# Optimization experiments

Hardware: AMD Instinct MI355X
Metric: run time of the kernel (lower is better)

## Reference

```python
import jax, jax.numpy as jnp
import numpy as np

BETA = 0.95
THR = 1.0
T = 50        # NUM_TIME_STEPS
L = 2         # SNN_NUM_LAYERS
SLOPE = 25.0  # fast_sigmoid surrogate slope

@jax.custom_vjp
def spike(v):
    # Heaviside on (mem - threshold) with fast_sigmoid surrogate gradient
    return (v > 0).astype(v.dtype)

def _spike_fwd(v):
    return (v > 0).astype(v.dtype), v

def _spike_bwd(v, g):
    return (g / (SLOPE * jnp.abs(v) + 1.0) ** 2,)

spike.defvjp(_spike_fwd, _spike_bwd)


def setup_inputs() -> dict:
    key = jax.random.key(0)
    k1, k2, _ = jax.random.split(key, 3)
    B, IN, H = 4096, 512, 1024
    x = jax.random.normal(k1, (B, IN), dtype=jnp.float32)
    W_proj = jax.random.normal(k2, (IN, H), dtype=jnp.float32) / np.sqrt(IN).astype(np.float32)
    b_proj = jnp.zeros((H,), dtype=jnp.float32)
    return {"x": x, "W_proj": W_proj, "b_proj": b_proj}


def reference(x, W_proj, b_proj):
    # Static input current fed at every time step (input_features != hidden -> Linear projection)
    inp = x @ W_proj + b_proj                         # [B, H]
    B, H = inp.shape

    def step(carry, _):
        mems, agg, tot = carry
        new_mems = []
        for li in range(L):  # independent LIF layers, all driven by the same static input
            mem = mems[li]
            # snnTorch Leaky (reset_mechanism='subtract'):
            reset = spike(mem - THR)                  # reset based on previous mem
            mem = BETA * mem + inp - reset * THR      # leaky integration + subtractive reset
            spk = spike(mem - THR)                    # output spike from new mem
            new_mems.append(mem)
            tot = tot + spk.sum(axis=1)               # total spikes per sample (all layers)
            if li == L - 1:
                agg = agg + spk                       # sum of last-layer spikes over time
        return (tuple(new_mems), agg, tot), None

    init = (
        tuple(jnp.zeros((B, H), inp.dtype) for _ in range(L)),  # init_leaky -> zeros
        jnp.zeros((B, H), inp.dtype),
        jnp.zeros((B,), inp.dtype),
    )
    (mems, agg, tot), _ = jax.lax.scan(step, init, None, length=T)
    return agg, tot
```

## Files before the change

kernel.cpp:

```cpp
#include <hip/hip_runtime.h>
#include <stdint.h>

#define MDIM 4096
#define NDIM 1024
#define KDIM 512
#define TSTEPS 50
#define NCH 16

typedef _Float16 half8 __attribute__((ext_vector_type(8)));
typedef float    f32x4 __attribute__((ext_vector_type(4)));

typedef const __attribute__((address_space(1))) void cgv_t;
typedef __attribute__((address_space(3))) void lv_t;

__device__ __forceinline__ void gload16(const void* g, void* s) {
    __builtin_amdgcn_global_load_lds((cgv_t*)g, (lv_t*)s, 16, 0, 0);
}

__global__ __launch_bounds__(256) void split_kernel(
    const float* __restrict__ A, const float* __restrict__ W,
    char* __restrict__ A1, char* __restrict__ A2,
    char* __restrict__ B1, char* __restrict__ B2,
    float* __restrict__ tot)
{
    const int blk = blockIdx.x;
    if (blk < 1024) {
        int idx = blk * 256 + threadIdx.x;
        if (idx < MDIM) tot[idx] = 0.0f;
        int r = idx >> 6, q = idx & 63, c = q >> 2, lg = q & 3;
        const float* pA = A + (size_t)r * KDIM + c * 32 + lg * 8;
        float4 v0 = *(const float4*)pA;
        float4 v1 = *(const float4*)(pA + 4);
        float v[8] = {v0.x, v0.y, v0.z, v0.w, v1.x, v1.y, v1.z, v1.w};
        half8 h1, h2;
        #pragma unroll
        for (int e = 0; e < 8; ++e) {
            h1[e] = (_Float16)v[e];
            h2[e] = (_Float16)((v[e] - (float)h1[e]) * 2048.0f);
        }
        int off = (r >> 6) * 65536 + c * 4096 + lg * 1024
                + (((r & 63) ^ (lg << 1)) << 4);
        *(half8*)(A1 + off) = h1;
        *(half8*)(A2 + off) = h2;
    } else {
        int idx = (blk - 1024) * 256 + threadIdx.x;
        int q = idx >> 10, n = idx & 1023, c = q >> 2, lg = q & 3;
        float v[8];
        #pragma unroll
        for (int e = 0; e < 8; ++e)
            v[e] = W[(size_t)(c * 32 + lg * 8 + e) * NDIM + n];
        half8 h1, h2;
        #pragma unroll
        for (int e = 0; e < 8; ++e) {
            h1[e] = (_Float16)v[e];
            h2[e] = (_Float16)((v[e] - (float)h1[e]) * 2048.0f);
        }
        int off = (n >> 6) * 65536 + c * 4096 + lg * 1024
                + (((n & 63) ^ (lg << 1)) << 4);
        *(half8*)(B1 + off) = h1;
        *(half8*)(B2 + off) = h2;
    }
}

__global__ __launch_bounds__(256, 4) void snn_mfma_kernel(
    const char* __restrict__ A1, const char* __restrict__ A2,
    const char* __restrict__ B1, const char* __restrict__ B2,
    const float* __restrict__ bias, float* __restrict__ agg, float* __restrict__ tot)
{
    __shared__ __align__(16) unsigned char lds[2][16384];

    const int t  = threadIdx.x;
    const int l  = t & 63;
    const int w  = t >> 6;
    const int li = l & 15;
    const int lg = l >> 4;
    const int qr = (w >> 1) * 32;
    const int qc = (w & 1) * 32;

    const int swz = (blockIdx.x & 7) * 128 + (blockIdx.x >> 3);
    const int m0 = (swz >> 4) * 64;
    const int n0 = (swz & 15) * 64;

    const int aoff = (m0 >> 6) * 65536 + w * 1024 + l * 16;
    const int boff = (n0 >> 6) * 65536 + w * 1024 + l * 16;
    const int dstw = w * 1024;

#define STAGE(buf, ch) do {                                                   \
    const int c_ = (ch) * 4096;                                               \
    gload16(A1 + aoff + c_, &lds[buf][dstw]);                                 \
    gload16(A2 + aoff + c_, &lds[buf][4096  + dstw]);                         \
    gload16(B1 + boff + c_, &lds[buf][8192  + dstw]);                         \
    gload16(B2 + boff + c_, &lds[buf][12288 + dstw]);                         \
} while (0)

    int aL[2], bL[2];
    #pragma unroll
    for (int i = 0; i < 2; ++i) {
        aL[i] = lg * 1024 + (((qr + i * 16 + li) ^ (lg << 1)) << 4);
        bL[i] = lg * 1024 + (((qc + i * 16 + li) ^ (lg << 1)) << 4);
    }

    f32x4 acc_lo[2][2], acc_hi[2][2];
    #pragma unroll
    for (int i = 0; i < 2; ++i)
        #pragma unroll
        for (int j = 0; j < 2; ++j) {
            acc_lo[i][j] = (f32x4){0.f, 0.f, 0.f, 0.f};
            acc_hi[i][j] = (f32x4){0.f, 0.f, 0.f, 0.f};
        }

    STAGE(0, 0);
    STAGE(1, 1);

    #pragma unroll 1
    for (int ch = 0; ch < NCH; ++ch) {
        if (ch < NCH - 1) asm volatile("s_waitcnt vmcnt(4)" ::: "memory");
        else              asm volatile("s_waitcnt vmcnt(0)" ::: "memory");
        __builtin_amdgcn_s_barrier();
        asm volatile("" ::: "memory");
        const unsigned char* sb = lds[ch & 1];

        half8 af1[2], af2[2], bf1[2], bf2[2];
        #pragma unroll
        for (int i = 0; i < 2; ++i) {
            af1[i] = *(const half8*)(sb + aL[i]);
            af2[i] = *(const half8*)(sb + 4096 + aL[i]);
            bf1[i] = *(const half8*)(sb + 8192 + bL[i]);
            bf2[i] = *(const half8*)(sb + 12288 + bL[i]);
        }
        #pragma unroll
        for (int i = 0; i < 2; ++i)
            #pragma unroll
            for (int j = 0; j < 2; ++j)
                acc_hi[i][j] = __builtin_amdgcn_mfma_f32_16x16x32_f16(
                    af2[i], bf1[j], acc_hi[i][j], 0, 0, 0);
        #pragma unroll
        for (int i = 0; i < 2; ++i)
            #pragma unroll
            for (int j = 0; j < 2; ++j)
                acc_hi[i][j] = __builtin_amdgcn_mfma_f32_16x16x32_f16(
                    af1[i], bf2[j], acc_hi[i][j], 0, 0, 0);
        #pragma unroll
        for (int i = 0; i < 2; ++i)
            #pragma unroll
            for (int j = 0; j < 2; ++j)
                acc_lo[i][j] = __builtin_amdgcn_mfma_f32_16x16x32_f16(
                    af1[i], bf1[j], acc_lo[i][j], 0, 0, 0);

        __builtin_amdgcn_s_barrier();
        asm volatile("" ::: "memory");
        if (ch + 2 < NCH) STAGE(ch & 1, ch + 2);
    }

    float cb[2];
    #pragma unroll
    for (int j = 0; j < 2; ++j) cb[j] = bias[n0 + qc + j * 16 + li];

    #pragma unroll
    for (int i = 0; i < 2; ++i) {
        int rsum[4] = {0, 0, 0, 0};
        #pragma unroll
        for (int j = 0; j < 2; ++j) {
            float c[4], c1[4], mem[4];
            int cnt[4];
            bool sp[4];
            #pragma unroll
            for (int r = 0; r < 4; ++r) {
                c[r]   = fmaf(acc_hi[i][j][r], 4.8828125e-4f, acc_lo[i][j][r])
                       + cb[j];
                c1[r]  = c[r] - 1.0f;
                mem[r] = 0.0f;
                cnt[r] = 0;
                sp[r]  = false;
            }
            #pragma unroll 1
            for (int tt = 0; tt < TSTEPS; ++tt) {
                #pragma unroll
                for (int r = 0; r < 4; ++r) {
                    mem[r] = fmaf(0.95f, mem[r], sp[r] ? c1[r] : c[r]);
                    sp[r]  = mem[r] > 1.0f;
                    cnt[r] += sp[r] ? 1 : 0;
                }
            }
            const int col = n0 + qc + j * 16 + li;
            #pragma unroll
            for (int r = 0; r < 4; ++r) {
                const int row = m0 + qr + i * 16 + lg * 4 + r;
                agg[(size_t)row * NDIM + col] = (float)cnt[r];
                rsum[r] += cnt[r];
            }
        }
        #pragma unroll
        for (int r = 0; r < 4; ++r) {
            int s = rsum[r];
            s += __shfl_xor(s, 1);
            s += __shfl_xor(s, 2);
            s += __shfl_xor(s, 4);
            s += __shfl_xor(s, 8);
            if (li == 0)
                atomicAdd(&tot[m0 + qr + i * 16 + lg * 4 + r], 2.0f * (float)s);
        }
        __builtin_amdgcn_sched_barrier(0);
    }
}

extern "C" void kernel_launch(void* const* d_in, const int* in_sizes, int n_in,
                              void* d_out, int out_size, void* d_ws, size_t ws_size,
                              hipStream_t stream) {
    const float* x = (const float*)d_in[0];
    const float* W = (const float*)d_in[1];
    const float* b = (const float*)d_in[2];
    float* agg = (float*)d_out;
    float* tot = agg + (size_t)MDIM * NDIM;

    char* ws = (char*)d_ws;
    char* A1 = ws;
    char* A2 = ws + (4 << 20);
    char* B1 = ws + (8 << 20);
    char* B2 = ws + (9 << 20);

    split_kernel<<<1024 + 256, 256, 0, stream>>>(x, W, A1, A2, B1, B2,
                                                 (float*)tot);
    snn_mfma_kernel<<<(MDIM / 64) * (NDIM / 64), 256, 0, stream>>>(
        A1, A2, B1, B2, b, agg, tot);
}
```

Measured before the change: 54.44 us.

## Switch to single-wave 32x32 tile blocks without barriers

```diff
diff --git a/kernel.cpp b/kernel.cpp
--- a/kernel.cpp
+++ b/kernel.cpp
@@ -38,8 +38,7 @@
             h1[e] = (_Float16)v[e];
             h2[e] = (_Float16)((v[e] - (float)h1[e]) * 2048.0f);
         }
-        int off = (r >> 6) * 65536 + c * 4096 + lg * 1024
-                + (((r & 63) ^ (lg << 1)) << 4);
+        int off = (r >> 5) * 32768 + c * 2048 + lg * 512 + ((r & 31) << 4);
         *(half8*)(A1 + off) = h1;
         *(half8*)(A2 + off) = h2;
     } else {
@@ -55,49 +54,50 @@
             h1[e] = (_Float16)v[e];
             h2[e] = (_Float16)((v[e] - (float)h1[e]) * 2048.0f);
         }
-        int off = (n >> 6) * 65536 + c * 4096 + lg * 1024
-                + (((n & 63) ^ (lg << 1)) << 4);
+        int off = (n >> 5) * 32768 + c * 2048 + lg * 512 + ((n & 31) << 4);
         *(half8*)(B1 + off) = h1;
         *(half8*)(B2 + off) = h2;
     }
 }
 
-__global__ __launch_bounds__(256, 4) void snn_mfma_kernel(
+__global__ __launch_bounds__(64) void snn_mfma_kernel(
     const char* __restrict__ A1, const char* __restrict__ A2,
     const char* __restrict__ B1, const char* __restrict__ B2,
     const float* __restrict__ bias, float* __restrict__ agg, float* __restrict__ tot)
 {
-    __shared__ __align__(16) unsigned char lds[2][16384];
-
-    const int t  = threadIdx.x;
-    const int l  = t & 63;
-    const int w  = t >> 6;
+    __shared__ __align__(16) unsigned char lds[2][8192];
+
+    const int l  = threadIdx.x;
     const int li = l & 15;
     const int lg = l >> 4;
-    const int qr = (w >> 1) * 32;
-    const int qc = (w & 1) * 32;
-
-    const int swz = (blockIdx.x & 7) * 128 + (blockIdx.x >> 3);
-    const int m0 = (swz >> 4) * 64;
-    const int n0 = (swz & 15) * 64;
-
-    const int aoff = (m0 >> 6) * 65536 + w * 1024 + l * 16;
-    const int boff = (n0 >> 6) * 65536 + w * 1024 + l * 16;
-    const int dstw = w * 1024;
+
+    const int swz = (blockIdx.x & 7) * 512 + (blockIdx.x >> 3);
+    const int m0 = (swz >> 5) * 32;
+    const int n0 = (swz & 31) * 32;
+
+    const char* a1p = A1 + (m0 >> 5) * 32768 + l * 16;
+    const char* a2p = A2 + (m0 >> 5) * 32768 + l * 16;
+    const char* b1p = B1 + (n0 >> 5) * 32768 + l * 16;
+    const char* b2p = B2 + (n0 >> 5) * 32768 + l * 16;
 
 #define STAGE(buf, ch) do {                                                   \
-    const int c_ = (ch) * 4096;                                               \
-    gload16(A1 + aoff + c_, &lds[buf][dstw]);                                 \
-    gload16(A2 + aoff + c_, &lds[buf][4096  + dstw]);                         \
-    gload16(B1 + boff + c_, &lds[buf][8192  + dstw]);                         \
-    gload16(B2 + boff + c_, &lds[buf][12288 + dstw]);                         \
+    const int c_ = (ch) * 2048;                                               \
+    unsigned char* lb_ = &lds[buf][0];                                        \
+    gload16(a1p + c_,        lb_);                                            \
+    gload16(a1p + c_ + 1024, lb_ + 1024);                                     \
+    gload16(a2p + c_,        lb_ + 2048);                                     \
+    gload16(a2p + c_ + 1024, lb_ + 3072);                                     \
+    gload16(b1p + c_,        lb_ + 4096);                                     \
+    gload16(b1p + c_ + 1024, lb_ + 5120);                                     \
+    gload16(b2p + c_,        lb_ + 6144);                                     \
+    gload16(b2p + c_ + 1024, lb_ + 7168);                                     \
 } while (0)
 
-    int aL[2], bL[2];
+    int aF[2], bF[2];
     #pragma unroll
     for (int i = 0; i < 2; ++i) {
-        aL[i] = lg * 1024 + (((qr + i * 16 + li) ^ (lg << 1)) << 4);
-        bL[i] = lg * 1024 + (((qc + i * 16 + li) ^ (lg << 1)) << 4);
+        aF[i] = lg * 512 + ((i * 16 + li) << 4);
+        bF[i] = lg * 512 + ((i * 16 + li) << 4);
     }
 
     f32x4 acc_lo[2][2], acc_hi[2][2];
@@ -114,19 +114,17 @@
 
     #pragma unroll 1
     for (int ch = 0; ch < NCH; ++ch) {
-        if (ch < NCH - 1) asm volatile("s_waitcnt vmcnt(4)" ::: "memory");
+        if (ch < NCH - 1) asm volatile("s_waitcnt vmcnt(8)" ::: "memory");
         else              asm volatile("s_waitcnt vmcnt(0)" ::: "memory");
-        __builtin_amdgcn_s_barrier();
-        asm volatile("" ::: "memory");
         const unsigned char* sb = lds[ch & 1];
 
         half8 af1[2], af2[2], bf1[2], bf2[2];
         #pragma unroll
         for (int i = 0; i < 2; ++i) {
-            af1[i] = *(const half8*)(sb + aL[i]);
-            af2[i] = *(const half8*)(sb + 4096 + aL[i]);
-            bf1[i] = *(const half8*)(sb + 8192 + bL[i]);
-            bf2[i] = *(const half8*)(sb + 12288 + bL[i]);
+            af1[i] = *(const half8*)(sb + aF[i]);
+            af2[i] = *(const half8*)(sb + 2048 + aF[i]);
+            bf1[i] = *(const half8*)(sb + 4096 + bF[i]);
+            bf2[i] = *(const half8*)(sb + 6144 + bF[i]);
         }
         #pragma unroll
         for (int i = 0; i < 2; ++i)
@@ -147,14 +145,15 @@
                 acc_lo[i][j] = __builtin_amdgcn_mfma_f32_16x16x32_f16(
                     af1[i], bf1[j], acc_lo[i][j], 0, 0, 0);
 
-        __builtin_amdgcn_s_barrier();
-        asm volatile("" ::: "memory");
-        if (ch + 2 < NCH) STAGE(ch & 1, ch + 2);
+        if (ch + 2 < NCH) {
+            asm volatile("s_waitcnt lgkmcnt(0)" ::: "memory");
+            STAGE(ch & 1, ch + 2);
+        }
     }
 
     float cb[2];
     #pragma unroll
-    for (int j = 0; j < 2; ++j) cb[j] = bias[n0 + qc + j * 16 + li];
+    for (int j = 0; j < 2; ++j) cb[j] = bias[n0 + j * 16 + li];
 
     #pragma unroll
     for (int i = 0; i < 2; ++i) {
@@ -182,10 +181,10 @@
                     cnt[r] += sp[r] ? 1 : 0;
                 }
             }
-            const int col = n0 + qc + j * 16 + li;
+            const int col = n0 + j * 16 + li;
             #pragma unroll
             for (int r = 0; r < 4; ++r) {
-                const int row = m0 + qr + i * 16 + lg * 4 + r;
+                const int row = m0 + i * 16 + lg * 4 + r;
                 agg[(size_t)row * NDIM + col] = (float)cnt[r];
                 rsum[r] += cnt[r];
             }
@@ -198,7 +197,7 @@
             s += __shfl_xor(s, 4);
             s += __shfl_xor(s, 8);
             if (li == 0)
-                atomicAdd(&tot[m0 + qr + i * 16 + lg * 4 + r], 2.0f * (float)s);
+                atomicAdd(&tot[m0 + i * 16 + lg * 4 + r], 2.0f * (float)s);
         }
         __builtin_amdgcn_sched_barrier(0);
     }
@@ -221,6 +220,6 @@
 
     split_kernel<<<1024 + 256, 256, 0, stream>>>(x, W, A1, A2, B1, B2,
                                                  (float*)tot);
-    snn_mfma_kernel<<<(MDIM / 64) * (NDIM / 64), 256, 0, stream>>>(
+    snn_mfma_kernel<<<(MDIM / 32) * (NDIM / 32), 64, 0, stream>>>(
         A1, A2, B1, B2, b, agg, tot);
 }
```

Measured after the change: 67.05 us. 1.23x slower.

## Replace LDS staging with direct register loads from fragment-packed global layout

Applied to the files above, without the earlier changes.

```diff
diff --git a/kernel.cpp b/kernel.cpp
--- a/kernel.cpp
+++ b/kernel.cpp
@@ -9,13 +9,6 @@
 
 typedef _Float16 half8 __attribute__((ext_vector_type(8)));
 typedef float    f32x4 __attribute__((ext_vector_type(4)));
-
-typedef const __attribute__((address_space(1))) void cgv_t;
-typedef __attribute__((address_space(3))) void lv_t;
-
-__device__ __forceinline__ void gload16(const void* g, void* s) {
-    __builtin_amdgcn_global_load_lds((cgv_t*)g, (lv_t*)s, 16, 0, 0);
-}
 
 __global__ __launch_bounds__(256) void split_kernel(
     const float* __restrict__ A, const float* __restrict__ W,
@@ -27,8 +20,8 @@
     if (blk < 1024) {
         int idx = blk * 256 + threadIdx.x;
         if (idx < MDIM) tot[idx] = 0.0f;
-        int r = idx >> 6, q = idx & 63, c = q >> 2, lg = q & 3;
-        const float* pA = A + (size_t)r * KDIM + c * 32 + lg * 8;
+        int r = idx >> 6, q = idx & 63;
+        const float* pA = A + (size_t)r * KDIM + q * 8;
         float4 v0 = *(const float4*)pA;
         float4 v1 = *(const float4*)(pA + 4);
         float v[8] = {v0.x, v0.y, v0.z, v0.w, v1.x, v1.y, v1.z, v1.w};
@@ -38,37 +31,35 @@
             h1[e] = (_Float16)v[e];
             h2[e] = (_Float16)((v[e] - (float)h1[e]) * 2048.0f);
         }
-        int off = (r >> 6) * 65536 + c * 4096 + lg * 1024
-                + (((r & 63) ^ (lg << 1)) << 4);
+        int off = ((r >> 4) * NCH + (q >> 2)) * 1024 + (q & 3) * 256
+                + (r & 15) * 16;
         *(half8*)(A1 + off) = h1;
         *(half8*)(A2 + off) = h2;
     } else {
         int idx = (blk - 1024) * 256 + threadIdx.x;
-        int q = idx >> 10, n = idx & 1023, c = q >> 2, lg = q & 3;
+        int q = idx >> 10, n = idx & 1023;
         float v[8];
         #pragma unroll
         for (int e = 0; e < 8; ++e)
-            v[e] = W[(size_t)(c * 32 + lg * 8 + e) * NDIM + n];
+            v[e] = W[(size_t)(q * 8 + e) * NDIM + n];
         half8 h1, h2;
         #pragma unroll
         for (int e = 0; e < 8; ++e) {
             h1[e] = (_Float16)v[e];
             h2[e] = (_Float16)((v[e] - (float)h1[e]) * 2048.0f);
         }
-        int off = (n >> 6) * 65536 + c * 4096 + lg * 1024
-                + (((n & 63) ^ (lg << 1)) << 4);
+        int off = ((n >> 4) * NCH + (q >> 2)) * 1024 + (q & 3) * 256
+                + (n & 15) * 16;
         *(half8*)(B1 + off) = h1;
         *(half8*)(B2 + off) = h2;
     }
 }
 
-__global__ __launch_bounds__(256, 4) void snn_mfma_kernel(
+__global__ __launch_bounds__(256, 3) void snn_mfma_kernel(
     const char* __restrict__ A1, const char* __restrict__ A2,
     const char* __restrict__ B1, const char* __restrict__ B2,
     const float* __restrict__ bias, float* __restrict__ agg, float* __restrict__ tot)
 {
-    __shared__ __align__(16) unsigned char lds[2][16384];
-
     const int t  = threadIdx.x;
     const int l  = t & 63;
     const int w  = t >> 6;
@@ -81,24 +72,34 @@
     const int m0 = (swz >> 4) * 64;
     const int n0 = (swz & 15) * 64;
 
-    const int aoff = (m0 >> 6) * 65536 + w * 1024 + l * 16;
-    const int boff = (n0 >> 6) * 65536 + w * 1024 + l * 16;
-    const int dstw = w * 1024;
-
-#define STAGE(buf, ch) do {                                                   \
-    const int c_ = (ch) * 4096;                                               \
-    gload16(A1 + aoff + c_, &lds[buf][dstw]);                                 \
-    gload16(A2 + aoff + c_, &lds[buf][4096  + dstw]);                         \
-    gload16(B1 + boff + c_, &lds[buf][8192  + dstw]);                         \
-    gload16(B2 + boff + c_, &lds[buf][12288 + dstw]);                         \
+    const char* pa1 = A1 + (size_t)(((m0 + qr) >> 4) * NCH) * 1024 + l * 16;
+    const char* pa2 = A2 + (size_t)(((m0 + qr) >> 4) * NCH) * 1024 + l * 16;
+    const char* pb1 = B1 + (size_t)(((n0 + qc) >> 4) * NCH) * 1024 + l * 16;
+    const char* pb2 = B2 + (size_t)(((n0 + qc) >> 4) * NCH) * 1024 + l * 16;
+
+#define LOADC(ch, Fa1, Fa2, Fb1, Fb2) do {                                    \
+    _Pragma("unroll") for (int i_ = 0; i_ < 2; ++i_) {                        \
+        Fa1[i_] = *(const half8*)(pa1 + (i_ * NCH + (ch)) * 1024);            \
+        Fa2[i_] = *(const half8*)(pa2 + (i_ * NCH + (ch)) * 1024);            \
+        Fb1[i_] = *(const half8*)(pb1 + (i_ * NCH + (ch)) * 1024);            \
+        Fb2[i_] = *(const half8*)(pb2 + (i_ * NCH + (ch)) * 1024);            \
+    }                                                                         \
 } while (0)
 
-    int aL[2], bL[2];
-    #pragma unroll
-    for (int i = 0; i < 2; ++i) {
-        aL[i] = lg * 1024 + (((qr + i * 16 + li) ^ (lg << 1)) << 4);
-        bL[i] = lg * 1024 + (((qc + i * 16 + li) ^ (lg << 1)) << 4);
-    }
+#define FMAC(Fa1, Fa2, Fb1, Fb2) do {                                        \
+    _Pragma("unroll") for (int i_ = 0; i_ < 2; ++i_)                          \
+        _Pragma("unroll") for (int j_ = 0; j_ < 2; ++j_)                      \
+            acc_hi[i_][j_] = __builtin_amdgcn_mfma_f32_16x16x32_f16(          \
+                Fa2[i_], Fb1[j_], acc_hi[i_][j_], 0, 0, 0);                   \
+    _Pragma("unroll") for (int i_ = 0; i_ < 2; ++i_)                          \
+        _Pragma("unroll") for (int j_ = 0; j_ < 2; ++j_)                      \
+            acc_hi[i_][j_] = __builtin_amdgcn_mfma_f32_16x16x32_f16(          \
+                Fa1[i_], Fb2[j_], acc_hi[i_][j_], 0, 0, 0);                   \
+    _Pragma("unroll") for (int i_ = 0; i_ < 2; ++i_)                          \
+        _Pragma("unroll") for (int j_ = 0; j_ < 2; ++j_)                      \
+            acc_lo[i_][j_] = __builtin_amdgcn_mfma_f32_16x16x32_f16(          \
+                Fa1[i_], Fb1[j_], acc_lo[i_][j_], 0, 0, 0);                   \
+} while (0)
 
     f32x4 acc_lo[2][2], acc_hi[2][2];
     #pragma unroll
@@ -109,48 +110,21 @@
             acc_hi[i][j] = (f32x4){0.f, 0.f, 0.f, 0.f};
         }
 
-    STAGE(0, 0);
-    STAGE(1, 1);
-
+    half8 Pa1[2], Pa2[2], Pb1[2], Pb2[2];
+    half8 Qa1[2], Qa2[2], Qb1[2], Qb2[2];
+
+    LOADC(0, Pa1, Pa2, Pb1, Pb2);
     #pragma unroll 1
-    for (int ch = 0; ch < NCH; ++ch) {
-        if (ch < NCH - 1) asm volatile("s_waitcnt vmcnt(4)" ::: "memory");
-        else              asm volatile("s_waitcnt vmcnt(0)" ::: "memory");
-        __builtin_amdgcn_s_barrier();
-        asm volatile("" ::: "memory");
-        const unsigned char* sb = lds[ch & 1];
-
-        half8 af1[2], af2[2], bf1[2], bf2[2];
-        #pragma unroll
-        for (int i = 0; i < 2; ++i) {
-            af1[i] = *(const half8*)(sb + aL[i]);
-            af2[i] = *(const half8*)(sb + 4096 + aL[i]);
-            bf1[i] = *(const half8*)(sb + 8192 + bL[i]);
-            bf2[i] = *(const half8*)(sb + 12288 + bL[i]);
-        }
-        #pragma unroll
-        for (int i = 0; i < 2; ++i)
-            #pragma unroll
-            for (int j = 0; j < 2; ++j)
-                acc_hi[i][j] = __builtin_amdgcn_mfma_f32_16x16x32_f16(
-                    af2[i], bf1[j], acc_hi[i][j], 0, 0, 0);
-        #pragma unroll
-        for (int i = 0; i < 2; ++i)
-            #pragma unroll
-            for (int j = 0; j < 2; ++j)
-                acc_hi[i][j] = __builtin_amdgcn_mfma_f32_16x16x32_f16(
-                    af1[i], bf2[j], acc_hi[i][j], 0, 0, 0);
-        #pragma unroll
-        for (int i = 0; i < 2; ++i)
-            #pragma unroll
-            for (int j = 0; j < 2; ++j)
-                acc_lo[i][j] = __builtin_amdgcn_mfma_f32_16x16x32_f16(
-                    af1[i], bf1[j], acc_lo[i][j], 0, 0, 0);
-
-        __builtin_amdgcn_s_barrier();
-        asm volatile("" ::: "memory");
-        if (ch + 2 < NCH) STAGE(ch & 1, ch + 2);
+    for (int tt = 0; tt < 7; ++tt) {
+        const int c0 = 2 * tt;
+        LOADC(c0 + 1, Qa1, Qa2, Qb1, Qb2);
+        FMAC(Pa1, Pa2, Pb1, Pb2);
+        LOADC(c0 + 2, Pa1, Pa2, Pb1, Pb2);
+        FMAC(Qa1, Qa2, Qb1, Qb2);
     }
+    LOADC(15, Qa1, Qa2, Qb1, Qb2);
+    FMAC(Pa1, Pa2, Pb1, Pb2);
+    FMAC(Qa1, Qa2, Qb1, Qb2);
 
     float cb[2];
     #pragma unroll
```

Result: slower. 58.79 us (+8.0%).

## Enlarge GEMM block tile to 128x128 with per-wave staging of split operands

Applied to the files above, without the earlier changes.

```diff
diff --git a/kernel.cpp b/kernel.cpp
--- a/kernel.cpp
+++ b/kernel.cpp
@@ -38,7 +38,7 @@
             h1[e] = (_Float16)v[e];
             h2[e] = (_Float16)((v[e] - (float)h1[e]) * 2048.0f);
         }
-        int off = (r >> 6) * 65536 + c * 4096 + lg * 1024
+        int off = ((r >> 6) * 16 + c) * 4096 + lg * 1024
                 + (((r & 63) ^ (lg << 1)) << 4);
         *(half8*)(A1 + off) = h1;
         *(half8*)(A2 + off) = h2;
@@ -55,56 +55,59 @@
             h1[e] = (_Float16)v[e];
             h2[e] = (_Float16)((v[e] - (float)h1[e]) * 2048.0f);
         }
-        int off = (n >> 6) * 65536 + c * 4096 + lg * 1024
+        int off = ((n >> 6) * 16 + c) * 4096 + lg * 1024
                 + (((n & 63) ^ (lg << 1)) << 4);
         *(half8*)(B1 + off) = h1;
         *(half8*)(B2 + off) = h2;
     }
 }
 
-__global__ __launch_bounds__(256, 4) void snn_mfma_kernel(
+__global__ __launch_bounds__(256, 2) void snn_mfma_kernel(
     const char* __restrict__ A1, const char* __restrict__ A2,
     const char* __restrict__ B1, const char* __restrict__ B2,
     const float* __restrict__ bias, float* __restrict__ agg, float* __restrict__ tot)
 {
-    __shared__ __align__(16) unsigned char lds[2][16384];
+    __shared__ __align__(16) unsigned char lds[2][32768];
 
     const int t  = threadIdx.x;
     const int l  = t & 63;
     const int w  = t >> 6;
     const int li = l & 15;
     const int lg = l >> 4;
-    const int qr = (w >> 1) * 32;
-    const int qc = (w & 1) * 32;
-
-    const int swz = (blockIdx.x & 7) * 128 + (blockIdx.x >> 3);
-    const int m0 = (swz >> 4) * 64;
-    const int n0 = (swz & 15) * 64;
-
-    const int aoff = (m0 >> 6) * 65536 + w * 1024 + l * 16;
-    const int boff = (n0 >> 6) * 65536 + w * 1024 + l * 16;
-    const int dstw = w * 1024;
+    const int qr = (w >> 1) * 64;
+    const int qc = (w & 1) * 64;
+
+    const int swz = (blockIdx.x & 7) * 32 + (blockIdx.x >> 3);
+    const int m0 = (swz >> 3) * 128;
+    const int n0 = (swz & 7) * 128;
+
+    const char* srcw = (w == 0) ? A1 : (w == 1) ? A2 : (w == 2) ? B1 : B2;
+    const int band0 = (w < 2) ? (m0 >> 6) : (n0 >> 6);
+    const int dstw  = w * 8192;
 
 #define STAGE(buf, ch) do {                                                   \
-    const int c_ = (ch) * 4096;                                               \
-    gload16(A1 + aoff + c_, &lds[buf][dstw]);                                 \
-    gload16(A2 + aoff + c_, &lds[buf][4096  + dstw]);                         \
-    gload16(B1 + boff + c_, &lds[buf][8192  + dstw]);                         \
-    gload16(B2 + boff + c_, &lds[buf][12288 + dstw]);                         \
+    _Pragma("unroll") for (int i_ = 0; i_ < 8; ++i_) {                        \
+        const int band_ = i_ >> 2, part_ = i_ & 3;                            \
+        gload16(srcw + (size_t)(((band0 + band_) * 16 + (ch)) * 4096          \
+                                + part_ * 1024 + l * 16),                     \
+                &lds[buf][dstw + band_ * 4096 + part_ * 1024]);               \
+    }                                                                         \
 } while (0)
 
-    int aL[2], bL[2];
-    #pragma unroll
-    for (int i = 0; i < 2; ++i) {
-        aL[i] = lg * 1024 + (((qr + i * 16 + li) ^ (lg << 1)) << 4);
-        bL[i] = lg * 1024 + (((qc + i * 16 + li) ^ (lg << 1)) << 4);
-    }
-
-    f32x4 acc_lo[2][2], acc_hi[2][2];
-    #pragma unroll
-    for (int i = 0; i < 2; ++i)
-        #pragma unroll
-        for (int j = 0; j < 2; ++j) {
+    const int abase = (w >> 1) * 4096;
+    const int bbase = (w & 1) * 4096;
+    int aF[4], bF[4];
+    #pragma unroll
+    for (int i = 0; i < 4; ++i) {
+        aF[i] = abase + lg * 1024 + (((i * 16 + li) ^ (lg << 1)) << 4);
+        bF[i] = bbase + lg * 1024 + (((i * 16 + li) ^ (lg << 1)) << 4);
+    }
+
+    f32x4 acc_lo[4][4], acc_hi[4][4];
+    #pragma unroll
+    for (int i = 0; i < 4; ++i)
+        #pragma unroll
+        for (int j = 0; j < 4; ++j) {
             acc_lo[i][j] = (f32x4){0.f, 0.f, 0.f, 0.f};
             acc_hi[i][j] = (f32x4){0.f, 0.f, 0.f, 0.f};
         }
@@ -114,36 +117,36 @@
 
     #pragma unroll 1
     for (int ch = 0; ch < NCH; ++ch) {
-        if (ch < NCH - 1) asm volatile("s_waitcnt vmcnt(4)" ::: "memory");
+        if (ch < NCH - 1) asm volatile("s_waitcnt vmcnt(8)" ::: "memory");
         else              asm volatile("s_waitcnt vmcnt(0)" ::: "memory");
         __builtin_amdgcn_s_barrier();
         asm volatile("" ::: "memory");
         const unsigned char* sb = lds[ch & 1];
 
-        half8 af1[2], af2[2], bf1[2], bf2[2];
-        #pragma unroll
-        for (int i = 0; i < 2; ++i) {
-            af1[i] = *(const half8*)(sb + aL[i]);
-            af2[i] = *(const half8*)(sb + 4096 + aL[i]);
-            bf1[i] = *(const half8*)(sb + 8192 + bL[i]);
-            bf2[i] = *(const half8*)(sb + 12288 + bL[i]);
-        }
-        #pragma unroll
-        for (int i = 0; i < 2; ++i)
-            #pragma unroll
-            for (int j = 0; j < 2; ++j)
+        half8 af1[4], af2[4], bf1[4], bf2[4];
+        #pragma unroll
+        for (int i = 0; i < 4; ++i) {
+            af1[i] = *(const half8*)(sb + aF[i]);
+            af2[i] = *(const half8*)(sb + 8192 + aF[i]);
+            bf1[i] = *(const half8*)(sb + 16384 + bF[i]);
+            bf2[i] = *(const half8*)(sb + 24576 + bF[i]);
+        }
+        #pragma unroll
+        for (int i = 0; i < 4; ++i)
+            #pragma unroll
+            for (int j = 0; j < 4; ++j)
                 acc_hi[i][j] = __builtin_amdgcn_mfma_f32_16x16x32_f16(
                     af2[i], bf1[j], acc_hi[i][j], 0, 0, 0);
         #pragma unroll
-        for (int i = 0; i < 2; ++i)
-            #pragma unroll
-            for (int j = 0; j < 2; ++j)
+        for (int i = 0; i < 4; ++i)
+            #pragma unroll
+            for (int j = 0; j < 4; ++j)
                 acc_hi[i][j] = __builtin_amdgcn_mfma_f32_16x16x32_f16(
                     af1[i], bf2[j], acc_hi[i][j], 0, 0, 0);
         #pragma unroll
-        for (int i = 0; i < 2; ++i)
-            #pragma unroll
-            for (int j = 0; j < 2; ++j)
+        for (int i = 0; i < 4; ++i)
+            #pragma unroll
+            for (int j = 0; j < 4; ++j)
                 acc_lo[i][j] = __builtin_amdgcn_mfma_f32_16x16x32_f16(
                     af1[i], bf1[j], acc_lo[i][j], 0, 0, 0);
 
@@ -152,15 +155,15 @@
         if (ch + 2 < NCH) STAGE(ch & 1, ch + 2);
     }
 
-    float cb[2];
-    #pragma unroll
-    for (int j = 0; j < 2; ++j) cb[j] = bias[n0 + qc + j * 16 + li];
-
-    #pragma unroll
-    for (int i = 0; i < 2; ++i) {
+    float cb[4];
+    #pragma unroll
+    for (int j = 0; j < 4; ++j) cb[j] = bias[n0 + qc + j * 16 + li];
+
+    #pragma unroll
+    for (int i = 0; i < 4; ++i) {
         int rsum[4] = {0, 0, 0, 0};
         #pragma unroll
-        for (int j = 0; j < 2; ++j) {
+        for (int j = 0; j < 4; ++j) {
             float c[4], c1[4], mem[4];
             int cnt[4];
             bool sp[4];
@@ -221,6 +224,6 @@
 
     split_kernel<<<1024 + 256, 256, 0, stream>>>(x, W, A1, A2, B1, B2,
                                                  (float*)tot);
-    snn_mfma_kernel<<<(MDIM / 64) * (NDIM / 64), 256, 0, stream>>>(
+    snn_mfma_kernel<<<(MDIM / 128) * (NDIM / 128), 256, 0, stream>>>(
         A1, A2, B1, B2, b, agg, tot);
 }
```

Measured after the change: 76.81 us. 41.1% more time.
